# Performance work log

Hardware: AMD Instinct MI355X
Metric: run time of the kernel (lower is better)

The kernel has to match this reference:

```python
import jax, jax.numpy as jnp
import numpy as np

TAU = 12.5        # from init_kwargs
THRESHOLD = 0.5   # from init_kwargs


def setup_inputs() -> dict:
    key = jax.random.key(0)
    stimulus = jax.random.normal(key, (4, 4096, 2048), dtype=jnp.float32)
    return {
        "stimulus": stimulus,
        "a": jnp.float32(0.7),   # nn.Parameter init 0.7
        "b": jnp.float32(0.8),   # nn.Parameter init 0.8
        "dt": jnp.float32(1.0),  # nn.Parameter init 1.0
        "n_steps": 8,
    }


def reference(stimulus, a, b, dt, n_steps):
    # Stimulus conditioning (matches torch forward exactly)
    stim_scale = jnp.clip(jnp.max(jnp.abs(stimulus), axis=-1, keepdims=True), 1e-6, None)
    stimulus_normed = stimulus / stim_scale
    threshold_gate = jax.nn.sigmoid((jnp.abs(stimulus) - THRESHOLD) * 10.0)
    I = stimulus_normed * (0.1 + 0.9 * threshold_gate)

    v = jnp.zeros_like(stimulus)
    w = jnp.zeros_like(stimulus)

    # IMEX FHN update loop (use_imex=True path). Note: the torch code computes an
    # intermediate w_new that is never used; only w_next (built from v_next) matters.
    alpha = dt / TAU
    denom = 1.0 + alpha * b
    for _ in range(n_steps):  # n_steps is a static Python int -> unrolled under jit
        dv_explicit = v - (v * v * v) / 3.0 - w + I
        v_next = v + dt * dv_explicit
        w_next = (w + alpha * (v_next + a)) / denom
        v = jnp.clip(v_next, -3.0, 3.0)
        w = jnp.clip(w_next, -3.0, 3.0)

    response = v * stim_scale
    return response, v
```

## Files before the change

kernel.cpp:

```cpp
#include <hip/hip_runtime.h>
#include <math.h>


#define ROWLEN 2048
#define BLOCK  256
#define EPT    8
#define F4PT   (EPT / 4)

__global__ __launch_bounds__(BLOCK)
void fhn_kernel(const float* __restrict__ stim,
                const float* __restrict__ a_p,
                const float* __restrict__ b_p,
                const float* __restrict__ dt_p,
                const int*   __restrict__ nsteps_p,
                float* __restrict__ out,
                long long n_elem)
{
    const long long row = blockIdx.x;
    const float* __restrict__ srow = stim + row * ROWLEN;
    float* __restrict__ rrow = out + row * ROWLEN;
    float* __restrict__ vrow = out + n_elem + row * ROWLEN;

    const int tid = threadIdx.x;

    float s[EPT];
    #pragma unroll
    for (int i = 0; i < F4PT; ++i) {
        float4 f = reinterpret_cast<const float4*>(srow)[tid + i * BLOCK];
        s[4*i+0] = f.x; s[4*i+1] = f.y; s[4*i+2] = f.z; s[4*i+3] = f.w;
    }

    float m = 0.0f;
    #pragma unroll
    for (int e = 0; e < EPT; ++e) m = fmaxf(m, fabsf(s[e]));
    #pragma unroll
    for (int off = 32; off > 0; off >>= 1)
        m = fmaxf(m, __shfl_xor(m, off, 64));
    __shared__ float smax[BLOCK / 64];
    if ((tid & 63) == 0) smax[tid >> 6] = m;
    __syncthreads();
    m = fmaxf(fmaxf(smax[0], smax[1]), fmaxf(smax[2], smax[3]));

    const float scale     = fmaxf(m, 1e-6f);
    const float inv_scale = 1.0f / scale;

    const float a  = *a_p;
    const float b  = *b_p;
    const float dt = *dt_p;
    const int   n_steps = *nsteps_p;
    const float alpha     = dt / 12.5f;
    const float inv_denom = 1.0f / (1.0f + alpha * b);

    const float c1 = 1.0f + dt;
    const float c2 = dt * (1.0f / 3.0f);
    const float kw = inv_denom;
    const float k1 = alpha * inv_denom;
    const float k2 = alpha * a * inv_denom;
    const float premul = dt * inv_scale;

    float dtI[EPT], v[EPT], w[EPT];
    #pragma unroll
    for (int e = 0; e < EPT; ++e) {
        const float as  = fabsf(s[e]);
        const float E   = __expf(fmaf(-10.0f, as, 5.0f));
        const float num = fmaf(0.1f, E, 1.0f);
        const float rd  = __builtin_amdgcn_rcpf(1.0f + E);
        dtI[e] = s[e] * premul * num * rd;
        v[e] = 0.0f;
        w[e] = 0.0f;
    }

    for (int n = 0; n < n_steps; ++n) {
        #pragma unroll
        for (int e = 0; e < EPT; ++e) {
            const float ve = v[e], we = w[e];
            const float t  = ve * ve;
            const float u  = fmaf(-dt, we, dtI[e]);
            const float p  = fmaf(c1, ve, u);
            const float q  = c2 * t;
            const float vn = fmaf(-q, ve, p);
            v[e] = fminf(fmaxf(vn, -3.0f), 3.0f);
            w[e] = fmaf(kw, we, fmaf(k1, vn, k2));
        }
    }

    #pragma unroll
    for (int i = 0; i < F4PT; ++i) {
        float4 r, vv;
        r.x  = v[4*i+0] * scale; r.y  = v[4*i+1] * scale;
        r.z  = v[4*i+2] * scale; r.w  = v[4*i+3] * scale;
        vv.x = v[4*i+0];         vv.y = v[4*i+1];
        vv.z = v[4*i+2];         vv.w = v[4*i+3];
        reinterpret_cast<float4*>(rrow)[tid + i * BLOCK] = r;
        reinterpret_cast<float4*>(vrow)[tid + i * BLOCK] = vv;
    }
}

extern "C" void kernel_launch(void* const* d_in, const int* in_sizes, int n_in,
                              void* d_out, int out_size, void* d_ws, size_t ws_size,
                              hipStream_t stream) {
    const float* stim = (const float*)d_in[0];
    const float* a_p  = (const float*)d_in[1];
    const float* b_p  = (const float*)d_in[2];
    const float* dt_p = (const float*)d_in[3];
    const int*   n_p  = (const int*)d_in[4];
    float* out = (float*)d_out;

    const long long n_elem = (long long)in_sizes[0];
    const int rows = (int)(n_elem / ROWLEN);
    if (rows <= 0) return;

    fhn_kernel<<<rows, BLOCK, 0, stream>>>(stim, a_p, b_p, dt_p, n_p, out, n_elem);
}
```

Before: 365.6 us.

## Use persistent blocks with next-row prefetch and double-buffered shared max

Replaces the one-block-per-row launch with a grid capped at 2048 blocks that loop over rows. Each block prefetches the next row's stimulus into registers while it computes the current one, so load latency overlaps compute. The __syncthreads is swapped for a raw barrier with a double-buffered shared max array. The aim is to cut block launch overhead and hide global-load latency, at the cost of higher register pressure and fewer resident blocks for latency hiding.

```diff
diff --git a/kernel.cpp b/kernel.cpp
--- a/kernel.cpp
+++ b/kernel.cpp
@@ -7,6 +7,8 @@
 #define EPT    8
 #define F4PT   (EPT / 4)
 
+typedef float vf4 __attribute__((ext_vector_type(4)));
+
 __global__ __launch_bounds__(BLOCK)
 void fhn_kernel(const float* __restrict__ stim,
                 const float* __restrict__ a_p,
@@ -14,35 +16,13 @@
                 const float* __restrict__ dt_p,
                 const int*   __restrict__ nsteps_p,
                 float* __restrict__ out,
-                long long n_elem)
+                long long n_elem, int rows)
 {
-    const long long row = blockIdx.x;
-    const float* __restrict__ srow = stim + row * ROWLEN;
-    float* __restrict__ rrow = out + row * ROWLEN;
-    float* __restrict__ vrow = out + n_elem + row * ROWLEN;
+    const int tid = threadIdx.x;
+    const int wid = tid >> 6;
+    const int G   = gridDim.x;
 
-    const int tid = threadIdx.x;
-
-    float s[EPT];
-    #pragma unroll
-    for (int i = 0; i < F4PT; ++i) {
-        float4 f = reinterpret_cast<const float4*>(srow)[tid + i * BLOCK];
-        s[4*i+0] = f.x; s[4*i+1] = f.y; s[4*i+2] = f.z; s[4*i+3] = f.w;
-    }
-
-    float m = 0.0f;
-    #pragma unroll
-    for (int e = 0; e < EPT; ++e) m = fmaxf(m, fabsf(s[e]));
-    #pragma unroll
-    for (int off = 32; off > 0; off >>= 1)
-        m = fmaxf(m, __shfl_xor(m, off, 64));
-    __shared__ float smax[BLOCK / 64];
-    if ((tid & 63) == 0) smax[tid >> 6] = m;
-    __syncthreads();
-    m = fmaxf(fmaxf(smax[0], smax[1]), fmaxf(smax[2], smax[3]));
-
-    const float scale     = fmaxf(m, 1e-6f);
-    const float inv_scale = 1.0f / scale;
+    __shared__ float smax[2][4];
 
     const float a  = *a_p;
     const float b  = *b_p;
@@ -50,49 +30,92 @@
     const int   n_steps = *nsteps_p;
     const float alpha     = dt / 12.5f;
     const float inv_denom = 1.0f / (1.0f + alpha * b);
-
     const float c1 = 1.0f + dt;
     const float c2 = dt * (1.0f / 3.0f);
     const float kw = inv_denom;
     const float k1 = alpha * inv_denom;
     const float k2 = alpha * a * inv_denom;
-    const float premul = dt * inv_scale;
 
-    float dtI[EPT], v[EPT], w[EPT];
-    #pragma unroll
-    for (int e = 0; e < EPT; ++e) {
-        const float as  = fabsf(s[e]);
-        const float E   = __expf(fmaf(-10.0f, as, 5.0f));
-        const float num = fmaf(0.1f, E, 1.0f);
-        const float rd  = __builtin_amdgcn_rcpf(1.0f + E);
-        dtI[e] = s[e] * premul * num * rd;
-        v[e] = 0.0f;
-        w[e] = 0.0f;
+    vf4 cur0, cur1, nxt0, nxt1;
+    {
+        const vf4* src = reinterpret_cast<const vf4*>(
+            stim + (long long)blockIdx.x * ROWLEN);
+        cur0 = src[tid];
+        cur1 = src[tid + BLOCK];
     }
 
-    for (int n = 0; n < n_steps; ++n) {
+    int it = 0;
+    for (int row = blockIdx.x; row < rows; row += G, ++it) {
+        const int nrow = row + G;
+        if (nrow < rows) {
+            const vf4* src = reinterpret_cast<const vf4*>(
+                stim + (long long)nrow * ROWLEN);
+            nxt0 = src[tid];
+            nxt1 = src[tid + BLOCK];
+        }
+
+        float m = fmaxf(fmaxf(fmaxf(fabsf(cur0.x), fabsf(cur0.y)),
+                              fmaxf(fabsf(cur0.z), fabsf(cur0.w))),
+                        fmaxf(fmaxf(fabsf(cur1.x), fabsf(cur1.y)),
+                              fmaxf(fabsf(cur1.z), fabsf(cur1.w))));
+        #pragma unroll
+        for (int off = 32; off > 0; off >>= 1)
+            m = fmaxf(m, __shfl_xor(m, off, 64));
+
+        const int p = it & 1;
+        if ((tid & 63) == 0) smax[p][wid] = m;
+        asm volatile("s_waitcnt lgkmcnt(0)" ::: "memory");
+        __builtin_amdgcn_s_barrier();
+        asm volatile("" ::: "memory");
+        m = fmaxf(fmaxf(smax[p][0], smax[p][1]),
+                  fmaxf(smax[p][2], smax[p][3]));
+
+        const float scale     = fmaxf(m, 1e-6f);
+        const float inv_scale = 1.0f / scale;
+        const float premul    = dt * inv_scale;
+
+        float s[EPT], dtI[EPT], v[EPT], w[EPT];
+        s[0]=cur0.x; s[1]=cur0.y; s[2]=cur0.z; s[3]=cur0.w;
+        s[4]=cur1.x; s[5]=cur1.y; s[6]=cur1.z; s[7]=cur1.w;
         #pragma unroll
         for (int e = 0; e < EPT; ++e) {
-            const float ve = v[e], we = w[e];
-            const float t  = ve * ve;
-            const float u  = fmaf(-dt, we, dtI[e]);
-            const float p  = fmaf(c1, ve, u);
-            const float q  = c2 * t;
-            const float vn = fmaf(-q, ve, p);
-            v[e] = fminf(fmaxf(vn, -3.0f), 3.0f);
-            w[e] = fmaf(kw, we, fmaf(k1, vn, k2));
+            const float as  = fabsf(s[e]);
+            const float E   = __expf(fmaf(-10.0f, as, 5.0f));
+            const float num = fmaf(0.1f, E, 1.0f);
+            const float rd  = __builtin_amdgcn_rcpf(1.0f + E);
+            dtI[e] = s[e] * premul * num * rd;
+            v[e] = 0.0f;
+            w[e] = 0.0f;
         }
-    }
 
-    #pragma unroll
-    for (int i = 0; i < F4PT; ++i) {
-        float4 r, vv;
-        r.x  = v[4*i+0] * scale; r.y  = v[4*i+1] * scale;
-        r.z  = v[4*i+2] * scale; r.w  = v[4*i+3] * scale;
-        vv.x = v[4*i+0];         vv.y = v[4*i+1];
-        vv.z = v[4*i+2];         vv.w = v[4*i+3];
-        reinterpret_cast<float4*>(rrow)[tid + i * BLOCK] = r;
-        reinterpret_cast<float4*>(vrow)[tid + i * BLOCK] = vv;
+        for (int n = 0; n < n_steps; ++n) {
+            #pragma unroll
+            for (int e = 0; e < EPT; ++e) {
+                const float ve = v[e], we = w[e];
+                const float t  = ve * ve;
+                const float u  = fmaf(-dt, we, dtI[e]);
+                const float pp = fmaf(c1, ve, u);
+                const float q  = c2 * t;
+                const float vn = fmaf(-q, ve, pp);
+                v[e] = fminf(fmaxf(vn, -3.0f), 3.0f);
+                w[e] = fmaf(kw, we, fmaf(k1, vn, k2));
+            }
+        }
+
+        float* rrow = out + (long long)row * ROWLEN;
+        float* vrow = out + n_elem + (long long)row * ROWLEN;
+        vf4 r0, r1, v0, v1;
+        r0.x = v[0]*scale; r0.y = v[1]*scale; r0.z = v[2]*scale; r0.w = v[3]*scale;
+        r1.x = v[4]*scale; r1.y = v[5]*scale; r1.z = v[6]*scale; r1.w = v[7]*scale;
+        v0.x = v[0]; v0.y = v[1]; v0.z = v[2]; v0.w = v[3];
+        v1.x = v[4]; v1.y = v[5]; v1.z = v[6]; v1.w = v[7];
+        reinterpret_cast<vf4*>(rrow)[tid]         = r0;
+        reinterpret_cast<vf4*>(rrow)[tid + BLOCK] = r1;
+        reinterpret_cast<vf4*>(vrow)[tid]         = v0;
+        reinterpret_cast<vf4*>(vrow)[tid + BLOCK] = v1;
+
+        cur0 = nxt0;
+        cur1 = nxt1;
     }
 }
 
@@ -110,5 +133,8 @@
     const int rows = (int)(n_elem / ROWLEN);
     if (rows <= 0) return;
 
-    fhn_kernel<<<rows, BLOCK, 0, stream>>>(stim, a_p, b_p, dt_p, n_p, out, n_elem);
+    int blocks = rows < 2048 ? rows : 2048;
+
+    fhn_kernel<<<blocks, BLOCK, 0, stream>>>(stim, a_p, b_p, dt_p, n_p,
+                                             out, n_elem, rows);
 }
```

Result: no change. 371.1 us (+1.5%).
